# Optimization experiments

Measured on AMD Instinct MI355X. Metric: run time of the kernel, lower is better.

Reference implementation:

```python
import jax, jax.numpy as jnp
import numpy as np

B, N = 64, 64
VOCAB, WORD_DIM = 10000, 512
NT, SEM = 30, 16


def _span_indices(n):
    # spans ordered by length k=1..n-1, within each k by left pos l=0..n-k-1
    ls = np.concatenate([np.arange(n - k) for k in range(1, n)])
    rs = np.concatenate([np.arange(n - k) + k for k in range(1, n)])
    return jnp.asarray(ls), jnp.asarray(rs)


def setup_inputs() -> dict:
    key = jax.random.key(0)
    k1, k2, k3, k4 = jax.random.split(key, 4)
    x = jax.random.randint(k1, (B, N), 0, VOCAB)
    lengths = jnp.full((B,), N, dtype=jnp.int64 if jax.config.read('jax_enable_x64') else jnp.int32)
    emb = jax.random.normal(k2, (VOCAB, WORD_DIM), dtype=jnp.float32) * 0.02
    # xavier-uniform for Linear(word_dim -> NT*SEM)
    lim = float(np.sqrt(6.0 / (WORD_DIM + NT * SEM)))
    w_out = jax.random.uniform(k3, (NT * SEM, WORD_DIM), minval=-lim, maxval=lim, dtype=jnp.float32)
    b_out = jnp.zeros((NT * SEM,), dtype=jnp.float32)
    return {"x": x, "lengths": lengths, "emb": emb, "w_out": w_out, "b_out": b_out}


def reference(x, lengths, emb, w_out, b_out):
    b, n = x.shape
    word_emb = emb[x]                                     # [b, N, word_dim]
    h = jnp.einsum('bnd,od->bno', word_emb, w_out) + b_out  # [b, N, NT*SEM]
    mask = (jnp.arange(n)[None, :] < lengths[:, None]).astype(h.dtype)
    wv = (h * mask[:, :, None]).reshape(b, n, NT, SEM)    # [b, N, NT, SEM]
    # prefix sums along sequence -> any contiguous span sum is one subtraction
    prefix = jnp.concatenate([jnp.zeros((b, 1, NT, SEM), h.dtype),
                              jnp.cumsum(wv, axis=1)], axis=1)  # [b, N+1, NT, SEM]
    ls, rs = _span_indices(n)                             # [N(N-1)/2]
    feats = prefix[:, rs + 1] - prefix[:, ls]             # span sums, [b, S, NT, SEM]
    norm = jnp.sqrt(jnp.sum(feats * feats, axis=-1, keepdims=True))
    return feats / norm
```

## Files before the change

kernel.cpp:

```cpp
#include <hip/hip_runtime.h>
#include <hip/hip_bf16.h>
#include <math.h>

#define BB 64
#define NN 64
#define WD 512
#define NTC 30
#define SEMD 16
#define OC 480
#define NSPAN 2016

typedef __bf16 bf16x8 __attribute__((ext_vector_type(8)));
typedef float floatx16 __attribute__((ext_vector_type(16)));

__global__ __launch_bounds__(256) void gemm_prefix_kernel(
    const int* __restrict__ x, const void* __restrict__ emb,
    const void* __restrict__ w, const void* __restrict__ bias,
    float* __restrict__ prefix)
{
    __shared__ float p[2][2][32][32];
    __shared__ float segsum[8][32];
    __shared__ int   sflags[2];

    const int tid  = threadIdx.x;
    const int wv   = tid >> 6;
    const int lane = tid & 63;
    const int b    = blockIdx.y;
    const int o0   = blockIdx.x * 32;

    if (tid < 2) sflags[tid] = 0;
    __syncthreads();
    {
        const __bf16* wb = (const __bf16*)w;
        float v = (float)wb[tid * 2];
        int huge = !(v > -1.0f && v < 1.0f);
        if (huge) atomicOr(&sflags[0], 1);
        if (tid == 0) {
            const int* xi0 = (const int*)x;
            int nz = 0;
            #pragma unroll
            for (int j = 1; j < 16; j += 2) nz |= xi0[j];
            if (nz == 0) sflags[1] = 1;
        }
    }
    __syncthreads();
    const int fp32mode = sflags[0];
    const int x64mode  = sflags[1];

    const int mtile = wv & 1;
    const int kh2   = wv >> 1;
    const int lrow  = lane & 31;
    const int khalf = lane >> 5;
    const int row   = b * 64 + mtile * 32 + lrow;
    const int col   = o0 + lrow;
    const int xi    = x64mode ? x[2 * row] : x[row];
    const int kbase = kh2 * 256 + khalf * 8;

    floatx16 acc = {};
    if (fp32mode) {
        const float* arow = (const float*)emb + (long)xi * WD + kbase;
        const float* brow = (const float*)w   + (long)col * WD + kbase;
        #pragma unroll 4
        for (int k = 0; k < 256; k += 16) {
            float4 a0 = *(const float4*)(arow + k);
            float4 a1 = *(const float4*)(arow + k + 4);
            float4 b0 = *(const float4*)(brow + k);
            float4 b1 = *(const float4*)(brow + k + 4);
            bf16x8 a, bv;
            a[0]=(__bf16)a0.x; a[1]=(__bf16)a0.y; a[2]=(__bf16)a0.z; a[3]=(__bf16)a0.w;
            a[4]=(__bf16)a1.x; a[5]=(__bf16)a1.y; a[6]=(__bf16)a1.z; a[7]=(__bf16)a1.w;
            bv[0]=(__bf16)b0.x; bv[1]=(__bf16)b0.y; bv[2]=(__bf16)b0.z; bv[3]=(__bf16)b0.w;
            bv[4]=(__bf16)b1.x; bv[5]=(__bf16)b1.y; bv[6]=(__bf16)b1.z; bv[7]=(__bf16)b1.w;
            acc = __builtin_amdgcn_mfma_f32_32x32x16_bf16(a, bv, acc, 0, 0, 0);
        }
    } else {
        const __bf16* arow = (const __bf16*)emb + (long)xi * WD + kbase;
        const __bf16* brow = (const __bf16*)w   + (long)col * WD + kbase;
        #pragma unroll 8
        for (int k = 0; k < 256; k += 16) {
            bf16x8 a = *(const bf16x8*)(arow + k);
            bf16x8 bv = *(const bf16x8*)(brow + k);
            acc = __builtin_amdgcn_mfma_f32_32x32x16_bf16(a, bv, acc, 0, 0, 0);
        }
    }

    #pragma unroll
    for (int r = 0; r < 16; ++r) {
        const int m = (r & 3) + 8 * (r >> 2) + 4 * khalf;
        p[mtile][kh2][m][lrow] = acc[r];
    }
    __syncthreads();

    const int o   = tid & 31;
    const int seg = tid >> 5;
    const float bo = fp32mode ? ((const float*)bias)[o0 + o]
                              : (float)((const __bf16*)bias)[o0 + o];
    float vals[8];
    float run = 0.f;
    #pragma unroll
    for (int j = 0; j < 8; ++j) {
        const int n  = seg * 8 + j;
        const int mt = n >> 5, mm = n & 31;
        float v = p[mt][0][mm][o] + p[mt][1][mm][o] + bo;
        vals[j] = v;
        run += v;
    }
    segsum[seg][o] = run;
    __syncthreads();

    float base = 0.f;
    #pragma unroll
    for (int j = 0; j < 7; ++j)
        if (j < seg) base += segsum[j][o];

    float* pref = prefix + ((long)b * 65) * OC + o0 + o;
    if (seg == 0) pref[0] = 0.f;
    float acc2 = base;
    #pragma unroll
    for (int j = 0; j < 8; ++j) {
        acc2 += vals[j];
        const int n = seg * 8 + j;
        pref[(long)(n + 1) * OC] = acc2;
    }
}

__global__ __launch_bounds__(256) void span_kernel(
    const float* __restrict__ prefix, float* __restrict__ out)
{
    const int tid  = threadIdx.x;
    const int g0   = blockIdx.x * 256;
    const int idx0 = g0 >> 2;
    const int t0   = idx0 / NTC;

    __shared__ int sl[4], sr[4], sb[4];
    if (tid < 4) {
        int t = t0 + tid;
        if (t > BB * NSPAN - 1) t = BB * NSPAN - 1;
        const int b = t / NSPAN;
        const int s = t - b * NSPAN;
        int k = (int)((127.0f - sqrtf(16129.0f - 8.0f * (float)s)) * 0.5f) + 1;
        while (64 * k - ((k * (k + 1)) >> 1) <= s) ++k;
        while (64 * (k - 1) - (((k - 1) * k) >> 1) > s) --k;
        const int fkm1 = 64 * (k - 1) - (((k - 1) * k) >> 1);
        const int l = s - fkm1;
        sl[tid] = l;
        sr[tid] = l + k + 1;
        sb[tid] = b;
    }
    __syncthreads();

    const int g   = g0 + tid;
    const int q   = g & 3;
    const int idx = g >> 2;
    const int nt  = idx % NTC;
    const int j   = idx / NTC - t0;
    const int l = sl[j], r = sr[j], b = sb[j];

    const long rowbase = ((long)b * 65) * OC + nt * SEMD + q * 4;
    const float4 a = *(const float4*)(prefix + rowbase + (long)l * OC);
    const float4 c = *(const float4*)(prefix + rowbase + (long)r * OC);

    float4 d;
    d.x = c.x - a.x; d.y = c.y - a.y; d.z = c.z - a.z; d.w = c.w - a.w;
    float ss = d.x * d.x + d.y * d.y + d.z * d.z + d.w * d.w;
    ss += __shfl_xor(ss, 1);
    ss += __shfl_xor(ss, 2);
    const float inv = rsqrtf(fmaxf(ss, 1e-30f));

    float4 v;
    v.x = d.x * inv; v.y = d.y * inv; v.z = d.z * inv; v.w = d.w * inv;
    *(float4*)(out + (long)g * 4) = v;
}

extern "C" void kernel_launch(void* const* d_in, const int* in_sizes, int n_in,
                              void* d_out, int out_size, void* d_ws, size_t ws_size,
                              hipStream_t stream) {
    const int*  x    = (const int*)d_in[0];
    const void* emb  = d_in[2];
    const void* w    = d_in[3];
    const void* bias = d_in[4];
    float*      out  = (float*)d_out;

    float* prefix = (float*)d_ws;

    gemm_prefix_kernel<<<dim3(15, BB), 256, 0, stream>>>(x, emb, w, bias, prefix);

    const int total4 = BB * NSPAN * NTC * 4;
    span_kernel<<<total4 / 256, 256, 0, stream>>>(prefix, out);
}
```

Baseline: 297.1 us.

## Stage gathered embedding rows in LDS and remap blocks for XCD locality

```diff
diff --git a/kernel.cpp b/kernel.cpp
--- a/kernel.cpp
+++ b/kernel.cpp
@@ -11,6 +11,7 @@
 #define NSPAN 2016
 
 typedef __bf16 bf16x8 __attribute__((ext_vector_type(8)));
+typedef __bf16 bf16x4 __attribute__((ext_vector_type(4)));
 typedef float floatx16 __attribute__((ext_vector_type(16)));
 
 __global__ __launch_bounds__(256) void gemm_prefix_kernel(
@@ -18,15 +19,23 @@
     const void* __restrict__ w, const void* __restrict__ bias,
     float* __restrict__ prefix)
 {
-    __shared__ float p[2][2][32][32];
-    __shared__ float segsum[8][32];
-    __shared__ int   sflags[2];
+    union SharedU {
+        __bf16 A[64][520];
+        struct { float p[2][2][32][32]; float segsum[8][32]; } e;
+    };
+    __shared__ SharedU sh;
+    __shared__ int sx[64];
+    __shared__ int sflags[2];
 
     const int tid  = threadIdx.x;
     const int wv   = tid >> 6;
     const int lane = tid & 63;
-    const int b    = blockIdx.y;
-    const int o0   = blockIdx.x * 32;
+
+    const int bid  = blockIdx.x;
+    const int xcd  = bid & 7;
+    const int slot = bid >> 3;
+    const int b    = xcd + ((slot / 15) << 3);
+    const int o0   = (slot % 15) * 32;
 
     if (tid < 2) sflags[tid] = 0;
     __syncthreads();
@@ -47,47 +56,69 @@
     const int fp32mode = sflags[0];
     const int x64mode  = sflags[1];
 
+    if (tid < 64) sx[tid] = x64mode ? x[2 * (b * 64 + tid)] : x[b * 64 + tid];
+    __syncthreads();
+
+    {
+        const int ar = tid >> 2, aq = tid & 3;
+        if (fp32mode) {
+            const float* src = (const float*)emb + (long)sx[ar] * WD;
+            #pragma unroll 8
+            for (int i = 0; i < 32; ++i) {
+                float4 t = *(const float4*)(src + aq * 4 + i * 16);
+                bf16x4 v;
+                v[0] = (__bf16)t.x; v[1] = (__bf16)t.y;
+                v[2] = (__bf16)t.z; v[3] = (__bf16)t.w;
+                *(bf16x4*)&sh.A[ar][aq * 4 + i * 16] = v;
+            }
+        } else {
+            const __bf16* src = (const __bf16*)emb + (long)sx[ar] * WD;
+            #pragma unroll 8
+            for (int i = 0; i < 16; ++i) {
+                *(bf16x8*)&sh.A[ar][aq * 8 + i * 32] =
+                    *(const bf16x8*)(src + aq * 8 + i * 32);
+            }
+        }
+    }
+    __syncthreads();
+
     const int mtile = wv & 1;
     const int kh2   = wv >> 1;
     const int lrow  = lane & 31;
     const int khalf = lane >> 5;
-    const int row   = b * 64 + mtile * 32 + lrow;
+    const int mrow  = mtile * 32 + lrow;
     const int col   = o0 + lrow;
-    const int xi    = x64mode ? x[2 * row] : x[row];
-    const int kbase = kh2 * 256 + khalf * 8;
+    const __bf16* aLds = &sh.A[mrow][kh2 * 256 + khalf * 8];
 
     floatx16 acc = {};
     if (fp32mode) {
-        const float* arow = (const float*)emb + (long)xi * WD + kbase;
-        const float* brow = (const float*)w   + (long)col * WD + kbase;
+        const float* brow = (const float*)w + (long)col * WD + kh2 * 256 + khalf * 8;
         #pragma unroll 4
-        for (int k = 0; k < 256; k += 16) {
-            float4 a0 = *(const float4*)(arow + k);
-            float4 a1 = *(const float4*)(arow + k + 4);
-            float4 b0 = *(const float4*)(brow + k);
-            float4 b1 = *(const float4*)(brow + k + 4);
-            bf16x8 a, bv;
-            a[0]=(__bf16)a0.x; a[1]=(__bf16)a0.y; a[2]=(__bf16)a0.z; a[3]=(__bf16)a0.w;
-            a[4]=(__bf16)a1.x; a[5]=(__bf16)a1.y; a[6]=(__bf16)a1.z; a[7]=(__bf16)a1.w;
+        for (int ks = 0; ks < 16; ++ks) {
+            float4 b0 = *(const float4*)(brow + ks * 16);
+            float4 b1 = *(const float4*)(brow + ks * 16 + 4);
+            bf16x8 a = *(const bf16x8*)(aLds + ks * 16);
+            bf16x8 bv;
             bv[0]=(__bf16)b0.x; bv[1]=(__bf16)b0.y; bv[2]=(__bf16)b0.z; bv[3]=(__bf16)b0.w;
             bv[4]=(__bf16)b1.x; bv[5]=(__bf16)b1.y; bv[6]=(__bf16)b1.z; bv[7]=(__bf16)b1.w;
             acc = __builtin_amdgcn_mfma_f32_32x32x16_bf16(a, bv, acc, 0, 0, 0);
         }
     } else {
-        const __bf16* arow = (const __bf16*)emb + (long)xi * WD + kbase;
-        const __bf16* brow = (const __bf16*)w   + (long)col * WD + kbase;
+        const __bf16* brow = (const __bf16*)w + (long)col * WD + kh2 * 256 + khalf * 8;
         #pragma unroll 8
-        for (int k = 0; k < 256; k += 16) {
-            bf16x8 a = *(const bf16x8*)(arow + k);
-            bf16x8 bv = *(const bf16x8*)(brow + k);
+        for (int ks = 0; ks < 16; ++ks) {
+            bf16x8 a  = *(const bf16x8*)(aLds + ks * 16);
+            bf16x8 bv = *(const bf16x8*)(brow + ks * 16);
             acc = __builtin_amdgcn_mfma_f32_32x32x16_bf16(a, bv, acc, 0, 0, 0);
         }
     }
+
+    __syncthreads();
 
     #pragma unroll
     for (int r = 0; r < 16; ++r) {
         const int m = (r & 3) + 8 * (r >> 2) + 4 * khalf;
-        p[mtile][kh2][m][lrow] = acc[r];
+        sh.e.p[mtile][kh2][m][lrow] = acc[r];
     }
     __syncthreads();
 
@@ -101,17 +132,17 @@
     for (int j = 0; j < 8; ++j) {
         const int n  = seg * 8 + j;
         const int mt = n >> 5, mm = n & 31;
-        float v = p[mt][0][mm][o] + p[mt][1][mm][o] + bo;
+        float v = sh.e.p[mt][0][mm][o] + sh.e.p[mt][1][mm][o] + bo;
         vals[j] = v;
         run += v;
     }
-    segsum[seg][o] = run;
+    sh.e.segsum[seg][o] = run;
     __syncthreads();
 
     float base = 0.f;
     #pragma unroll
     for (int j = 0; j < 7; ++j)
-        if (j < seg) base += segsum[j][o];
+        if (j < seg) base += sh.e.segsum[j][o];
 
     float* pref = prefix + ((long)b * 65) * OC + o0 + o;
     if (seg == 0) pref[0] = 0.f;
@@ -183,7 +214,7 @@
 
     float* prefix = (float*)d_ws;
 
-    gemm_prefix_kernel<<<dim3(15, BB), 256, 0, stream>>>(x, emb, w, bias, prefix);
+    gemm_prefix_kernel<<<960, 256, 0, stream>>>(x, emb, w, bias, prefix);
 
     const int total4 = BB * NSPAN * NTC * 4;
     span_kernel<<<total4 / 256, 256, 0, stream>>>(prefix, out);
```

After: 289.0 us. 1.03x faster.
